# Kernel optimization log

Measured on AMD Instinct MI355X. Metric: run time of the kernel, lower is better.

## Reference

```python
import jax, jax.numpy as jnp
import numpy as np

B = 64            # batch size (number of segments)
PTS = 4096        # points per segment
N = B * PTS       # total points
OBS = 128
ACT = 5
HID = 256
LAT = 64
CTX = 128
TEMP = 1.0
LOG2PIE = float(np.log(2.0 * np.pi * np.e))


def _p(key, shape, scale=0.02):
    return (scale * jax.random.normal(key, shape)).astype(jnp.float32)


def setup_inputs() -> dict:
    key = jax.random.key(0)
    ks = jax.random.split(key, 20)
    inp = {
        'obs': jax.random.normal(ks[0], (N, OBS), dtype=jnp.float32),
        'action': jax.random.normal(ks[1], (B, ACT), dtype=jnp.float32),
        'coh_scalar': jax.random.normal(ks[2], (B, 1), dtype=jnp.float32),
        'coh_spatial': jax.random.normal(ks[3], (N,), dtype=jnp.float32),
        'h_prev': jnp.zeros((B, HID), jnp.float32),
        'z_prev': jnp.zeros((B, LAT), jnp.float32),
        'batch': jnp.repeat(jnp.arange(B, dtype=jnp.int64), PTS),
    }
    xin = LAT + ACT + 1  # GRU input: [z_prev, action, coh_scalar]
    inp['W_ih'] = _p(ks[4], (3 * HID, xin)); inp['b_ih'] = jnp.zeros((3 * HID,), jnp.float32)
    inp['W_hh'] = _p(ks[5], (3 * HID, HID)); inp['b_hh'] = jnp.zeros((3 * HID,), jnp.float32)
    inp['W_prior'] = _p(ks[6], (2 * LAT, HID)); inp['b_prior'] = jnp.zeros((2 * LAT,), jnp.float32)
    inp['W_post'] = _p(ks[7], (2 * LAT, HID + OBS)); inp['b_post'] = jnp.zeros((2 * LAT,), jnp.float32)
    inp['W_ae1'] = _p(ks[8], (256, OBS)); inp['b_ae1'] = jnp.zeros((256,), jnp.float32)
    inp['W_ae2'] = _p(ks[9], (OBS, 256)); inp['b_ae2'] = jnp.zeros((OBS,), jnp.float32)
    inp['W_c1'] = _p(ks[10], (512, HID + LAT + OBS)); inp['b_c1'] = jnp.zeros((512,), jnp.float32)
    inp['W_c2'] = _p(ks[11], (CTX, 512)); inp['b_c2'] = jnp.zeros((CTX,), jnp.float32)
    return inp


def _forward(obs, action, coh_scalar, coh_spatial, h_prev, z_prev, batch,
             W_ih, b_ih, W_hh, b_hh, W_prior, b_prior, W_post, b_post,
             W_ae1, b_ae1, W_ae2, b_ae2, W_c1, b_c1, W_c2, b_c2):
    # --- segment mean of obs (the hot scatter-reduce) ---
    counts = jax.ops.segment_sum(jnp.ones((N,), obs.dtype), batch, num_segments=B)
    obs_sum = jax.ops.segment_sum(obs, batch, num_segments=B)            # (B, OBS)
    obs_agg = obs_sum / jnp.maximum(counts, 1.0)[:, None]

    # --- RSSM: GRU cell over [z_prev, action, coh_scalar] ---
    x = jnp.concatenate([z_prev, action, coh_scalar], axis=-1)           # (B, LAT+ACT+1)
    gi = x @ W_ih.T + b_ih
    gh = h_prev @ W_hh.T + b_hh
    gi_r, gi_z, gi_n = jnp.split(gi, 3, axis=-1)
    gh_r, gh_z, gh_n = jnp.split(gh, 3, axis=-1)
    r = jax.nn.sigmoid(gi_r + gh_r)
    u = jax.nn.sigmoid(gi_z + gh_z)
    n = jnp.tanh(gi_n + r * gh_n)
    h = (1.0 - u) * n + u * h_prev                                       # (B, HID)

    prior = h @ W_prior.T + b_prior
    mu_p, logvar_p = jnp.split(prior, 2, axis=-1)
    post = jnp.concatenate([h, obs_agg], axis=-1) @ W_post.T + b_post
    mu_q, logvar_q = jnp.split(post, 2, axis=-1)
    z = mu_q                                                             # deterministic baseline (B, LAT)

    # --- priority: entropy-based uncertainty, per-segment softmax ---
    uncertainty = 0.5 * jnp.sum(logvar_q + LOG2PIE, axis=-1)             # (B,)
    priority = coh_spatial * uncertainty[batch]                          # (N,)
    s = priority / TEMP
    m = jax.ops.segment_max(s, batch, num_segments=B)
    e = jnp.exp(s - m[batch])
    denom = jax.ops.segment_sum(e, batch, num_segments=B)
    priority_norm = e / jnp.maximum(denom, 1e-12)[batch]                 # (N,)

    # --- attended aggregation (second scatter-reduce) ---
    obs_attended = jax.ops.segment_sum(obs * priority_norm[:, None], batch, num_segments=B)  # (B, OBS)
    obs_enc = jax.nn.relu(obs_attended @ W_ae1.T + b_ae1) @ W_ae2.T + b_ae2                  # (B, OBS)

    ctx_in = jnp.concatenate([h, z, obs_enc], axis=-1)                   # (B, HID+LAT+OBS)
    context = jax.nn.relu(ctx_in @ W_c1.T + b_c1) @ W_c2.T + b_c2        # (B, CTX)
    return h, z, context, priority, priority_norm, uncertainty


def reference(obs, action, coh_scalar, coh_spatial, h_prev, z_prev, batch,
              W_ih, b_ih, W_hh, b_hh, W_prior, b_prior, W_post, b_post,
              W_ae1, b_ae1, W_ae2, b_ae2, W_c1, b_c1, W_c2, b_c2):
    return _forward(obs, action, coh_scalar, coh_spatial, h_prev, z_prev, batch,
                    W_ih, b_ih, W_hh, b_hh, W_prior, b_prior, W_post, b_post,
                    W_ae1, b_ae1, W_ae2, b_ae2, W_c1, b_c1, W_c2, b_c2)
```

## Files before the change

### kernel.cpp

```cpp
#include <hip/hip_runtime.h>
#include <math.h>

#define BB   64
#define PTS  4096
#define NTOT (BB * PTS)
#define OBS  128
#define ACT  5
#define HID  256
#define LAT  64
#define CTX  128
#define LOG2PIE 2.8378770664093453f

#define OFF_H   0
#define OFF_Z   (BB * HID)
#define OFF_CTX (OFF_Z + BB * LAT)
#define OFF_PRI (OFF_CTX + BB * CTX)
#define OFF_PN  (OFF_PRI + NTOT)
#define OFF_UNC (OFF_PN + NTOT)

#define CHUNKS 32
#define RPC    (PTS / CHUNKS)

__device__ __forceinline__ float wsum(float v) {
    #pragma unroll
    for (int off = 32; off > 0; off >>= 1) v += __shfl_xor(v, off, 64);
    return v;
}
__device__ __forceinline__ float wmax(float v) {
    #pragma unroll
    for (int off = 32; off > 0; off >>= 1) v = fmaxf(v, __shfl_xor(v, off, 64));
    return v;
}
__device__ __forceinline__ float sigmoidf_(float x) { return 1.f / (1.f + expf(-x)); }

__global__ __launch_bounds__(256) void seg_sum_part_kernel(
        const float* __restrict__ obs, float* __restrict__ part) {
    int blk = blockIdx.x;
    int b = blk >> 5, chunk = blk & 31;
    int t = threadIdx.x, c4 = t & 31, rg = t >> 5;
    const float4* obs4 = (const float4*)obs;
    size_t row0 = (size_t)b * PTS + (size_t)chunk * RPC;
    float4 acc = make_float4(0.f, 0.f, 0.f, 0.f);
    #pragma unroll
    for (int i = 0; i < RPC / 8; ++i) {
        float4 v = obs4[(row0 + rg + 8 * i) * (OBS / 4) + c4];
        acc.x += v.x; acc.y += v.y; acc.z += v.z; acc.w += v.w;
    }
    __shared__ float4 lds[256];
    lds[t] = acc;
    __syncthreads();
    if (t < 32) {
        float4 s = lds[t];
        #pragma unroll
        for (int k = 1; k < 8; ++k) {
            float4 v = lds[t + 32 * k];
            s.x += v.x; s.y += v.y; s.z += v.z; s.w += v.w;
        }
        ((float4*)part)[(size_t)blk * 32 + t] = s;
    }
}

__global__ __launch_bounds__(256) void attn_part_kernel(
        const float* __restrict__ obs, const float* __restrict__ pn,
        float* __restrict__ att_part) {
    int blk = blockIdx.x;
    int b = blk >> 5, chunk = blk & 31;
    int t = threadIdx.x, c4 = t & 31, rg = t >> 5;
    const float4* obs4 = (const float4*)obs;
    size_t row0 = (size_t)b * PTS + (size_t)chunk * RPC;
    float4 acc = make_float4(0.f, 0.f, 0.f, 0.f);
    #pragma unroll
    for (int i = 0; i < RPC / 8; ++i) {
        size_t r = row0 + rg + 8 * i;
        float w = pn[r];
        float4 v = obs4[r * (OBS / 4) + c4];
        acc.x = fmaf(v.x, w, acc.x);
        acc.y = fmaf(v.y, w, acc.y);
        acc.z = fmaf(v.z, w, acc.z);
        acc.w = fmaf(v.w, w, acc.w);
    }
    __shared__ float4 lds[256];
    lds[t] = acc;
    __syncthreads();
    if (t < 32) {
        float4 s = lds[t];
        #pragma unroll
        for (int k = 1; k < 8; ++k) {
            float4 v = lds[t + 32 * k];
            s.x += v.x; s.y += v.y; s.z += v.z; s.w += v.w;
        }
        ((float4*)att_part)[(size_t)blk * 32 + t] = s;
    }
}

__global__ __launch_bounds__(128) void agg_kernel(const float* __restrict__ part,
                                                  float* __restrict__ agg,
                                                  float* __restrict__ out) {
    int b = blockIdx.x, j = threadIdx.x;
    float s = 0.f;
    #pragma unroll
    for (int c = 0; c < CHUNKS; ++c) s += part[((size_t)b * CHUNKS + c) * OBS + j];
    agg[b * OBS + j] = s * (1.0f / PTS);
    if (j == 0) out[OFF_UNC + b] = 32.0f * LOG2PIE;
}

__global__ __launch_bounds__(128) void attagg_kernel(const float* __restrict__ att_part,
                                                     float* __restrict__ att) {
    int b = blockIdx.x, j = threadIdx.x;
    float s = 0.f;
    #pragma unroll
    for (int c = 0; c < CHUNKS; ++c) s += att_part[((size_t)b * CHUNKS + c) * OBS + j];
    att[b * OBS + j] = s;
}

__global__ __launch_bounds__(256) void gru_gate_kernel(
        const float* __restrict__ action, const float* __restrict__ coh_scalar,
        const float* __restrict__ h_prev, const float* __restrict__ z_prev,
        const float* __restrict__ W_ih, const float* __restrict__ b_ih,
        const float* __restrict__ W_hh, const float* __restrict__ b_hh,
        float* __restrict__ out) {
    int wid = blockIdx.x * 4 + (threadIdx.x >> 6);
    int lane = threadIdx.x & 63;
    int b = wid >> 8, j = wid & 255;

    float x0 = z_prev[b * LAT + lane];
    float x1 = 0.f;
    if (lane < ACT) x1 = action[b * ACT + lane];
    else if (lane == ACT) x1 = coh_scalar[b];
    float hp0 = h_prev[b * HID + lane];
    float hp1 = h_prev[b * HID + lane + 64];
    float hp2 = h_prev[b * HID + lane + 128];
    float hp3 = h_prev[b * HID + lane + 192];

    const float* wir = W_ih + (size_t)j * 70;
    const float* wiz = W_ih + (size_t)(HID + j) * 70;
    const float* win = W_ih + (size_t)(2 * HID + j) * 70;
    const float* whr = W_hh + (size_t)j * HID;
    const float* whz = W_hh + (size_t)(HID + j) * HID;
    const float* whn = W_hh + (size_t)(2 * HID + j) * HID;

    float sr = wir[lane] * x0;
    float sz = wiz[lane] * x0;
    float sn = win[lane] * x0;
    if (lane < 6) {
        sr = fmaf(wir[lane + 64], x1, sr);
        sz = fmaf(wiz[lane + 64], x1, sz);
        sn = fmaf(win[lane + 64], x1, sn);
    }
    sr = fmaf(whr[lane], hp0, sr); sr = fmaf(whr[lane + 64], hp1, sr);
    sr = fmaf(whr[lane + 128], hp2, sr); sr = fmaf(whr[lane + 192], hp3, sr);
    sz = fmaf(whz[lane], hp0, sz); sz = fmaf(whz[lane + 64], hp1, sz);
    sz = fmaf(whz[lane + 128], hp2, sz); sz = fmaf(whz[lane + 192], hp3, sz);
    float sh = whn[lane] * hp0;
    sh = fmaf(whn[lane + 64], hp1, sh);
    sh = fmaf(whn[lane + 128], hp2, sh);
    sh = fmaf(whn[lane + 192], hp3, sh);

    sr = wsum(sr); sz = wsum(sz); sn = wsum(sn); sh = wsum(sh);
    if (lane == 0) {
        float r = sigmoidf_(sr + b_ih[j] + b_hh[j]);
        float u = sigmoidf_(sz + b_ih[HID + j] + b_hh[HID + j]);
        float n = tanhf(sn + b_ih[2 * HID + j] + r * (sh + b_hh[2 * HID + j]));
        float h = (1.f - u) * n + u * h_prev[b * HID + j];
        out[OFF_H + b * HID + j] = h;
    }
}

__global__ __launch_bounds__(256) void post_kernel(
        const float* __restrict__ agg,
        const float* __restrict__ W_post, const float* __restrict__ b_post,
        float* __restrict__ out) {
    int wid = blockIdx.x * 4 + (threadIdx.x >> 6);
    int lane = threadIdx.x & 63;
    int b = wid >> 7, row = wid & 127;
    const float* wr = W_post + (size_t)row * (HID + OBS);
    const float* h = out + OFF_H + b * HID;
    const float* ag = agg + b * OBS;
    float s = wr[lane] * h[lane];
    s = fmaf(wr[lane + 64], h[lane + 64], s);
    s = fmaf(wr[lane + 128], h[lane + 128], s);
    s = fmaf(wr[lane + 192], h[lane + 192], s);
    s = fmaf(wr[lane + 256], ag[lane], s);
    s = fmaf(wr[lane + 320], ag[lane + 64], s);
    s = wsum(s);
    if (lane == 0) {
        s += b_post[row];
        if (row < LAT) out[OFF_Z + b * LAT + row] = s;
        else atomicAdd(&out[OFF_UNC + b], 0.5f * s);
    }
}

__global__ __launch_bounds__(1024) void softmax_kernel(
        const float* __restrict__ coh_spatial, float* __restrict__ out) {
    int b = blockIdx.x, t = threadIdx.x;
    int w = t >> 6, lane = t & 63;
    float u = out[OFF_UNC + b];
    __shared__ float sv[PTS];
    __shared__ float red[16];
    int base = b * PTS;
    float lmax = -INFINITY;
    #pragma unroll
    for (int i = t; i < PTS; i += 1024) {
        float s = coh_spatial[base + i] * u;
        sv[i] = s;
        out[OFF_PRI + base + i] = s;
        lmax = fmaxf(lmax, s);
    }
    lmax = wmax(lmax);
    if (lane == 0) red[w] = lmax;
    __syncthreads();
    float m = red[0];
    #pragma unroll
    for (int k = 1; k < 16; ++k) m = fmaxf(m, red[k]);
    __syncthreads();
    float lsum = 0.f;
    #pragma unroll
    for (int i = t; i < PTS; i += 1024) {
        float e = expf(sv[i] - m);
        sv[i] = e;
        lsum += e;
    }
    lsum = wsum(lsum);
    if (lane == 0) red[w] = lsum;
    __syncthreads();
    float d = 0.f;
    #pragma unroll
    for (int k = 0; k < 16; ++k) d += red[k];
    float inv = 1.f / fmaxf(d, 1e-12f);
    #pragma unroll
    for (int i = t; i < PTS; i += 1024) {
        out[OFF_PN + base + i] = sv[i] * inv;
    }
}

__global__ __launch_bounds__(256) void ae1_kernel(
        const float* __restrict__ att,
        const float* __restrict__ W_ae1, const float* __restrict__ b_ae1,
        float* __restrict__ h1) {
    int wid = blockIdx.x * 4 + (threadIdx.x >> 6);
    int lane = threadIdx.x & 63;
    int b = wid >> 8, row = wid & 255;
    const float* wr = W_ae1 + (size_t)row * OBS;
    const float* a = att + b * OBS;
    float s = wr[lane] * a[lane];
    s = fmaf(wr[lane + 64], a[lane + 64], s);
    s = wsum(s);
    if (lane == 0) h1[b * 256 + row] = fmaxf(s + b_ae1[row], 0.f);
}

__global__ __launch_bounds__(256) void ae2_kernel(
        const float* __restrict__ h1,
        const float* __restrict__ W_ae2, const float* __restrict__ b_ae2,
        float* __restrict__ enc) {
    int wid = blockIdx.x * 4 + (threadIdx.x >> 6);
    int lane = threadIdx.x & 63;
    int b = wid >> 7, row = wid & 127;
    const float* wr = W_ae2 + (size_t)row * 256;
    const float* hh = h1 + b * 256;
    float s = wr[lane] * hh[lane];
    s = fmaf(wr[lane + 64], hh[lane + 64], s);
    s = fmaf(wr[lane + 128], hh[lane + 128], s);
    s = fmaf(wr[lane + 192], hh[lane + 192], s);
    s = wsum(s);
    if (lane == 0) enc[b * OBS + row] = s + b_ae2[row];
}

__global__ __launch_bounds__(256) void c1_kernel(
        const float* __restrict__ enc,
        const float* __restrict__ W_c1, const float* __restrict__ b_c1,
        const float* __restrict__ out, float* __restrict__ c1v) {
    int wid = blockIdx.x * 4 + (threadIdx.x >> 6);
    int lane = threadIdx.x & 63;
    int b = wid >> 9, row = wid & 511;
    const float* wr = W_c1 + (size_t)row * 448;
    const float* h = out + OFF_H + b * HID;
    const float* z = out + OFF_Z + b * LAT;
    const float* e = enc + b * OBS;
    float s = wr[lane] * h[lane];
    s = fmaf(wr[lane + 64], h[lane + 64], s);
    s = fmaf(wr[lane + 128], h[lane + 128], s);
    s = fmaf(wr[lane + 192], h[lane + 192], s);
    s = fmaf(wr[lane + 256], z[lane], s);
    s = fmaf(wr[lane + 320], e[lane], s);
    s = fmaf(wr[lane + 384], e[lane + 64], s);
    s = wsum(s);
    if (lane == 0) c1v[b * 512 + row] = fmaxf(s + b_c1[row], 0.f);
}

__global__ __launch_bounds__(256) void c2_kernel(
        const float* __restrict__ c1v,
        const float* __restrict__ W_c2, const float* __restrict__ b_c2,
        float* __restrict__ out) {
    int wid = blockIdx.x * 4 + (threadIdx.x >> 6);
    int lane = threadIdx.x & 63;
    int b = wid >> 7, row = wid & 127;
    const float* wr = W_c2 + (size_t)row * 512;
    const float* c = c1v + b * 512;
    float s = wr[lane] * c[lane];
    #pragma unroll
    for (int i = 1; i < 8; ++i) s = fmaf(wr[lane + 64 * i], c[lane + 64 * i], s);
    s = wsum(s);
    if (lane == 0) out[OFF_CTX + b * CTX + row] = s + b_c2[row];
}

extern "C" void kernel_launch(void* const* d_in, const int* in_sizes, int n_in,
                              void* d_out, int out_size, void* d_ws, size_t ws_size,
                              hipStream_t stream) {
    const float* obs         = (const float*)d_in[0];
    const float* action      = (const float*)d_in[1];
    const float* coh_scalar  = (const float*)d_in[2];
    const float* coh_spatial = (const float*)d_in[3];
    const float* h_prev      = (const float*)d_in[4];
    const float* z_prev      = (const float*)d_in[5];
    const float* W_ih   = (const float*)d_in[7];
    const float* b_ih   = (const float*)d_in[8];
    const float* W_hh   = (const float*)d_in[9];
    const float* b_hh   = (const float*)d_in[10];
    const float* W_post = (const float*)d_in[13];
    const float* b_post = (const float*)d_in[14];
    const float* W_ae1  = (const float*)d_in[15];
    const float* b_ae1  = (const float*)d_in[16];
    const float* W_ae2  = (const float*)d_in[17];
    const float* b_ae2  = (const float*)d_in[18];
    const float* W_c1   = (const float*)d_in[19];
    const float* b_c1   = (const float*)d_in[20];
    const float* W_c2   = (const float*)d_in[21];
    const float* b_c2   = (const float*)d_in[22];

    float* out = (float*)d_out;
    float* part     = (float*)d_ws;
    float* att_part = part + BB * CHUNKS * OBS;
    float* agg      = att_part + BB * CHUNKS * OBS;
    float* att      = agg + BB * OBS;
    float* h1       = att + BB * OBS;
    float* enc      = h1 + BB * 256;
    float* c1v      = enc + BB * OBS;

    seg_sum_part_kernel<<<BB * CHUNKS, 256, 0, stream>>>(obs, part);
    gru_gate_kernel<<<BB * HID / 4, 256, 0, stream>>>(action, coh_scalar, h_prev, z_prev,
                                                      W_ih, b_ih, W_hh, b_hh, out);
    agg_kernel<<<BB, 128, 0, stream>>>(part, agg, out);
    post_kernel<<<BB * 128 / 4, 256, 0, stream>>>(agg, W_post, b_post, out);
    softmax_kernel<<<BB, 1024, 0, stream>>>(coh_spatial, out);
    attn_part_kernel<<<BB * CHUNKS, 256, 0, stream>>>(obs, out + OFF_PN, att_part);
    attagg_kernel<<<BB, 128, 0, stream>>>(att_part, att);
    ae1_kernel<<<BB * 256 / 4, 256, 0, stream>>>(att, W_ae1, b_ae1, h1);
    ae2_kernel<<<BB * 128 / 4, 256, 0, stream>>>(h1, W_ae2, b_ae2, enc);
    c1_kernel<<<BB * 512 / 4, 256, 0, stream>>>(enc, W_c1, b_c1, out, c1v);
    c2_kernel<<<BB * 128 / 4, 256, 0, stream>>>(c1v, W_c2, b_c2, out);
}
```

Baseline: 314.5 us.

## Fuse kernels: merge seg-sum with GRU, agg into post, MLP head into one kernel

Cuts the chain from eleven launches to five. The segment-sum partials and the GRU gate now run as one horizontally fused launch, and the chunk reduction is folded into post_kernel. The uncertainty atomicAdd is replaced by a per-batch log-variance buffer that softmax_kernel reduces. The attended reduction and the four MLP layers (ae1, ae2, c1, c2) run in a single 1024-thread block per batch with shared-memory intermediates. This removes launch and sync overhead and global round trips, but the fused head uses only 64 blocks, and each block streams all of the weights.

Result: faster. 295.3 us (-6.1%).

```diff
diff --git a/kernel.cpp b/kernel.cpp
--- a/kernel.cpp
+++ b/kernel.cpp
@@ -33,30 +33,194 @@
 }
 __device__ __forceinline__ float sigmoidf_(float x) { return 1.f / (1.f + expf(-x)); }
 
-__global__ __launch_bounds__(256) void seg_sum_part_kernel(
-        const float* __restrict__ obs, float* __restrict__ part) {
+__global__ __launch_bounds__(256) void phase1_kernel(
+        const float* __restrict__ obs, float* __restrict__ part,
+        const float* __restrict__ action, const float* __restrict__ coh_scalar,
+        const float* __restrict__ h_prev, const float* __restrict__ z_prev,
+        const float* __restrict__ W_ih, const float* __restrict__ b_ih,
+        const float* __restrict__ W_hh, const float* __restrict__ b_hh,
+        float* __restrict__ out) {
+    __shared__ float4 lds[256];
+    int t = threadIdx.x;
+    if (blockIdx.x < BB * CHUNKS) {
+        int blk = blockIdx.x;
+        int b = blk >> 5, chunk = blk & 31;
+        int c4 = t & 31, rg = t >> 5;
+        const float4* obs4 = (const float4*)obs;
+        size_t row0 = (size_t)b * PTS + (size_t)chunk * RPC;
+        float4 acc = make_float4(0.f, 0.f, 0.f, 0.f);
+        #pragma unroll
+        for (int i = 0; i < RPC / 8; ++i) {
+            float4 v = obs4[(row0 + rg + 8 * i) * (OBS / 4) + c4];
+            acc.x += v.x; acc.y += v.y; acc.z += v.z; acc.w += v.w;
+        }
+        lds[t] = acc;
+        __syncthreads();
+        if (t < 32) {
+            float4 s = lds[t];
+            #pragma unroll
+            for (int k = 1; k < 8; ++k) {
+                float4 v = lds[t + 32 * k];
+                s.x += v.x; s.y += v.y; s.z += v.z; s.w += v.w;
+            }
+            ((float4*)part)[(size_t)blk * 32 + t] = s;
+        }
+    } else {
+        int wid = (blockIdx.x - BB * CHUNKS) * 4 + (t >> 6);
+        int lane = t & 63;
+        int b = wid >> 8, j = wid & 255;
+
+        float x0 = z_prev[b * LAT + lane];
+        float x1 = 0.f;
+        if (lane < ACT) x1 = action[b * ACT + lane];
+        else if (lane == ACT) x1 = coh_scalar[b];
+        float hp0 = h_prev[b * HID + lane];
+        float hp1 = h_prev[b * HID + lane + 64];
+        float hp2 = h_prev[b * HID + lane + 128];
+        float hp3 = h_prev[b * HID + lane + 192];
+
+        const float* wir = W_ih + (size_t)j * 70;
+        const float* wiz = W_ih + (size_t)(HID + j) * 70;
+        const float* win = W_ih + (size_t)(2 * HID + j) * 70;
+        const float* whr = W_hh + (size_t)j * HID;
+        const float* whz = W_hh + (size_t)(HID + j) * HID;
+        const float* whn = W_hh + (size_t)(2 * HID + j) * HID;
+
+        float sr = wir[lane] * x0;
+        float sz = wiz[lane] * x0;
+        float sn = win[lane] * x0;
+        if (lane < 6) {
+            sr = fmaf(wir[lane + 64], x1, sr);
+            sz = fmaf(wiz[lane + 64], x1, sz);
+            sn = fmaf(win[lane + 64], x1, sn);
+        }
+        sr = fmaf(whr[lane], hp0, sr); sr = fmaf(whr[lane + 64], hp1, sr);
+        sr = fmaf(whr[lane + 128], hp2, sr); sr = fmaf(whr[lane + 192], hp3, sr);
+        sz = fmaf(whz[lane], hp0, sz); sz = fmaf(whz[lane + 64], hp1, sz);
+        sz = fmaf(whz[lane + 128], hp2, sz); sz = fmaf(whz[lane + 192], hp3, sz);
+        float sh = whn[lane] * hp0;
+        sh = fmaf(whn[lane + 64], hp1, sh);
+        sh = fmaf(whn[lane + 128], hp2, sh);
+        sh = fmaf(whn[lane + 192], hp3, sh);
+
+        sr = wsum(sr); sz = wsum(sz); sn = wsum(sn); sh = wsum(sh);
+        if (lane == 0) {
+            float r = sigmoidf_(sr + b_ih[j] + b_hh[j]);
+            float u = sigmoidf_(sz + b_ih[HID + j] + b_hh[HID + j]);
+            float n = tanhf(sn + b_ih[2 * HID + j] + r * (sh + b_hh[2 * HID + j]));
+            float h = (1.f - u) * n + u * h_prev[b * HID + j];
+            out[OFF_H + b * HID + j] = h;
+        }
+    }
+}
+
+__global__ __launch_bounds__(256) void post_kernel(
+        const float* __restrict__ part,
+        const float* __restrict__ W_post, const float* __restrict__ b_post,
+        float* __restrict__ out, float* __restrict__ lv) {
     int blk = blockIdx.x;
-    int b = blk >> 5, chunk = blk & 31;
-    int t = threadIdx.x, c4 = t & 31, rg = t >> 5;
-    const float4* obs4 = (const float4*)obs;
-    size_t row0 = (size_t)b * PTS + (size_t)chunk * RPC;
-    float4 acc = make_float4(0.f, 0.f, 0.f, 0.f);
-    #pragma unroll
-    for (int i = 0; i < RPC / 8; ++i) {
-        float4 v = obs4[(row0 + rg + 8 * i) * (OBS / 4) + c4];
-        acc.x += v.x; acc.y += v.y; acc.z += v.z; acc.w += v.w;
-    }
-    __shared__ float4 lds[256];
-    lds[t] = acc;
+    int b = blk >> 5, rg = blk & 31;
+    int t = threadIdx.x, w = t >> 6, lane = t & 63;
+    __shared__ float4 st[256];
+    __shared__ float aggs[128];
+    __shared__ float hs[256];
+
+    const float4* ap4 = (const float4*)part;
+    {
+        int c4 = t & 31, cg = t >> 5;
+        float4 a = ap4[((size_t)(b * CHUNKS + cg)) * 32 + c4];
+        #pragma unroll
+        for (int k = 1; k < 4; ++k) {
+            float4 v = ap4[((size_t)(b * CHUNKS + cg + 8 * k)) * 32 + c4];
+            a.x += v.x; a.y += v.y; a.z += v.z; a.w += v.w;
+        }
+        st[t] = a;
+    }
+    hs[t] = out[OFF_H + b * HID + t];
     __syncthreads();
     if (t < 32) {
-        float4 s = lds[t];
+        float4 s = st[t];
         #pragma unroll
         for (int k = 1; k < 8; ++k) {
-            float4 v = lds[t + 32 * k];
+            float4 v = st[t + 32 * k];
             s.x += v.x; s.y += v.y; s.z += v.z; s.w += v.w;
         }
-        ((float4*)part)[(size_t)blk * 32 + t] = s;
+        const float sc = 1.0f / PTS;
+        aggs[4 * t + 0] = s.x * sc;
+        aggs[4 * t + 1] = s.y * sc;
+        aggs[4 * t + 2] = s.z * sc;
+        aggs[4 * t + 3] = s.w * sc;
+    }
+    __syncthreads();
+
+    int row = rg * 4 + w;
+    const float* wr = W_post + (size_t)row * (HID + OBS);
+    float s = wr[lane] * hs[lane];
+    s = fmaf(wr[lane + 64],  hs[lane + 64],  s);
+    s = fmaf(wr[lane + 128], hs[lane + 128], s);
+    s = fmaf(wr[lane + 192], hs[lane + 192], s);
+    s = fmaf(wr[lane + 256], aggs[lane],      s);
+    s = fmaf(wr[lane + 320], aggs[lane + 64], s);
+    s = wsum(s);
+    if (lane == 0) {
+        s += b_post[row];
+        if (row < LAT) out[OFF_Z + b * LAT + row] = s;
+        else           lv[b * LAT + (row - LAT)] = s;
+    }
+}
+
+__global__ __launch_bounds__(1024) void softmax_kernel(
+        const float* __restrict__ coh_spatial, const float* __restrict__ lv,
+        float* __restrict__ out) {
+    int b = blockIdx.x, t = threadIdx.x;
+    int w = t >> 6, lane = t & 63;
+    __shared__ float sv[PTS];
+    __shared__ float red[16];
+    __shared__ float uS;
+    if (w == 0) {
+        float v = lv[b * LAT + lane];
+        v = wsum(v);
+        if (lane == 0) {
+            float u = 0.5f * v + 32.0f * LOG2PIE;
+            uS = u;
+            out[OFF_UNC + b] = u;
+        }
+    }
+    __syncthreads();
+    float u = uS;
+    int base = b * PTS;
+    float lmax = -INFINITY;
+    #pragma unroll
+    for (int i = t; i < PTS; i += 1024) {
+        float s = coh_spatial[base + i] * u;
+        sv[i] = s;
+        out[OFF_PRI + base + i] = s;
+        lmax = fmaxf(lmax, s);
+    }
+    lmax = wmax(lmax);
+    if (lane == 0) red[w] = lmax;
+    __syncthreads();
+    float m = red[0];
+    #pragma unroll
+    for (int k = 1; k < 16; ++k) m = fmaxf(m, red[k]);
+    __syncthreads();
+    float lsum = 0.f;
+    #pragma unroll
+    for (int i = t; i < PTS; i += 1024) {
+        float e = expf(sv[i] - m);
+        sv[i] = e;
+        lsum += e;
+    }
+    lsum = wsum(lsum);
+    if (lane == 0) red[w] = lsum;
+    __syncthreads();
+    float d = 0.f;
+    #pragma unroll
+    for (int k = 0; k < 16; ++k) d += red[k];
+    float inv = 1.f / fmaxf(d, 1e-12f);
+    #pragma unroll
+    for (int i = t; i < PTS; i += 1024) {
+        out[OFF_PN + base + i] = sv[i] * inv;
     }
 }
 
@@ -72,12 +236,12 @@
     #pragma unroll
     for (int i = 0; i < RPC / 8; ++i) {
         size_t r = row0 + rg + 8 * i;
-        float w = pn[r];
+        float wgt = pn[r];
         float4 v = obs4[r * (OBS / 4) + c4];
-        acc.x = fmaf(v.x, w, acc.x);
-        acc.y = fmaf(v.y, w, acc.y);
-        acc.z = fmaf(v.z, w, acc.z);
-        acc.w = fmaf(v.w, w, acc.w);
+        acc.x = fmaf(v.x, wgt, acc.x);
+        acc.y = fmaf(v.y, wgt, acc.y);
+        acc.z = fmaf(v.z, wgt, acc.z);
+        acc.w = fmaf(v.w, wgt, acc.w);
     }
     __shared__ float4 lds[256];
     lds[t] = acc;
@@ -93,214 +257,164 @@
     }
 }
 
-__global__ __launch_bounds__(128) void agg_kernel(const float* __restrict__ part,
-                                                  float* __restrict__ agg,
-                                                  float* __restrict__ out) {
-    int b = blockIdx.x, j = threadIdx.x;
-    float s = 0.f;
-    #pragma unroll
-    for (int c = 0; c < CHUNKS; ++c) s += part[((size_t)b * CHUNKS + c) * OBS + j];
-    agg[b * OBS + j] = s * (1.0f / PTS);
-    if (j == 0) out[OFF_UNC + b] = 32.0f * LOG2PIE;
-}
-
-__global__ __launch_bounds__(128) void attagg_kernel(const float* __restrict__ att_part,
-                                                     float* __restrict__ att) {
-    int b = blockIdx.x, j = threadIdx.x;
-    float s = 0.f;
-    #pragma unroll
-    for (int c = 0; c < CHUNKS; ++c) s += att_part[((size_t)b * CHUNKS + c) * OBS + j];
-    att[b * OBS + j] = s;
-}
-
-__global__ __launch_bounds__(256) void gru_gate_kernel(
-        const float* __restrict__ action, const float* __restrict__ coh_scalar,
-        const float* __restrict__ h_prev, const float* __restrict__ z_prev,
-        const float* __restrict__ W_ih, const float* __restrict__ b_ih,
-        const float* __restrict__ W_hh, const float* __restrict__ b_hh,
+__global__ __launch_bounds__(1024) void head_kernel(
+        const float* __restrict__ att_part,
+        const float* __restrict__ W_ae1, const float* __restrict__ b_ae1,
+        const float* __restrict__ W_ae2, const float* __restrict__ b_ae2,
+        const float* __restrict__ W_c1,  const float* __restrict__ b_c1,
+        const float* __restrict__ W_c2,  const float* __restrict__ b_c2,
         float* __restrict__ out) {
-    int wid = blockIdx.x * 4 + (threadIdx.x >> 6);
-    int lane = threadIdx.x & 63;
-    int b = wid >> 8, j = wid & 255;
-
-    float x0 = z_prev[b * LAT + lane];
-    float x1 = 0.f;
-    if (lane < ACT) x1 = action[b * ACT + lane];
-    else if (lane == ACT) x1 = coh_scalar[b];
-    float hp0 = h_prev[b * HID + lane];
-    float hp1 = h_prev[b * HID + lane + 64];
-    float hp2 = h_prev[b * HID + lane + 128];
-    float hp3 = h_prev[b * HID + lane + 192];
-
-    const float* wir = W_ih + (size_t)j * 70;
-    const float* wiz = W_ih + (size_t)(HID + j) * 70;
-    const float* win = W_ih + (size_t)(2 * HID + j) * 70;
-    const float* whr = W_hh + (size_t)j * HID;
-    const float* whz = W_hh + (size_t)(HID + j) * HID;
-    const float* whn = W_hh + (size_t)(2 * HID + j) * HID;
-
-    float sr = wir[lane] * x0;
-    float sz = wiz[lane] * x0;
-    float sn = win[lane] * x0;
-    if (lane < 6) {
-        sr = fmaf(wir[lane + 64], x1, sr);
-        sz = fmaf(wiz[lane + 64], x1, sz);
-        sn = fmaf(win[lane + 64], x1, sn);
-    }
-    sr = fmaf(whr[lane], hp0, sr); sr = fmaf(whr[lane + 64], hp1, sr);
-    sr = fmaf(whr[lane + 128], hp2, sr); sr = fmaf(whr[lane + 192], hp3, sr);
-    sz = fmaf(whz[lane], hp0, sz); sz = fmaf(whz[lane + 64], hp1, sz);
-    sz = fmaf(whz[lane + 128], hp2, sz); sz = fmaf(whz[lane + 192], hp3, sz);
-    float sh = whn[lane] * hp0;
-    sh = fmaf(whn[lane + 64], hp1, sh);
-    sh = fmaf(whn[lane + 128], hp2, sh);
-    sh = fmaf(whn[lane + 192], hp3, sh);
-
-    sr = wsum(sr); sz = wsum(sz); sn = wsum(sn); sh = wsum(sh);
-    if (lane == 0) {
-        float r = sigmoidf_(sr + b_ih[j] + b_hh[j]);
-        float u = sigmoidf_(sz + b_ih[HID + j] + b_hh[HID + j]);
-        float n = tanhf(sn + b_ih[2 * HID + j] + r * (sh + b_hh[2 * HID + j]));
-        float h = (1.f - u) * n + u * h_prev[b * HID + j];
-        out[OFF_H + b * HID + j] = h;
-    }
-}
-
-__global__ __launch_bounds__(256) void post_kernel(
-        const float* __restrict__ agg,
-        const float* __restrict__ W_post, const float* __restrict__ b_post,
-        float* __restrict__ out) {
-    int wid = blockIdx.x * 4 + (threadIdx.x >> 6);
-    int lane = threadIdx.x & 63;
-    int b = wid >> 7, row = wid & 127;
-    const float* wr = W_post + (size_t)row * (HID + OBS);
-    const float* h = out + OFF_H + b * HID;
-    const float* ag = agg + b * OBS;
-    float s = wr[lane] * h[lane];
-    s = fmaf(wr[lane + 64], h[lane + 64], s);
-    s = fmaf(wr[lane + 128], h[lane + 128], s);
-    s = fmaf(wr[lane + 192], h[lane + 192], s);
-    s = fmaf(wr[lane + 256], ag[lane], s);
-    s = fmaf(wr[lane + 320], ag[lane + 64], s);
-    s = wsum(s);
-    if (lane == 0) {
-        s += b_post[row];
-        if (row < LAT) out[OFF_Z + b * LAT + row] = s;
-        else atomicAdd(&out[OFF_UNC + b], 0.5f * s);
-    }
-}
-
-__global__ __launch_bounds__(1024) void softmax_kernel(
-        const float* __restrict__ coh_spatial, float* __restrict__ out) {
     int b = blockIdx.x, t = threadIdx.x;
     int w = t >> 6, lane = t & 63;
-    float u = out[OFF_UNC + b];
-    __shared__ float sv[PTS];
-    __shared__ float red[16];
-    int base = b * PTS;
-    float lmax = -INFINITY;
-    #pragma unroll
-    for (int i = t; i < PTS; i += 1024) {
-        float s = coh_spatial[base + i] * u;
-        sv[i] = s;
-        out[OFF_PRI + base + i] = s;
-        lmax = fmaxf(lmax, s);
-    }
-    lmax = wmax(lmax);
-    if (lane == 0) red[w] = lmax;
-    __syncthreads();
-    float m = red[0];
-    #pragma unroll
-    for (int k = 1; k < 16; ++k) m = fmaxf(m, red[k]);
-    __syncthreads();
-    float lsum = 0.f;
-    #pragma unroll
-    for (int i = t; i < PTS; i += 1024) {
-        float e = expf(sv[i] - m);
-        sv[i] = e;
-        lsum += e;
-    }
-    lsum = wsum(lsum);
-    if (lane == 0) red[w] = lsum;
-    __syncthreads();
-    float d = 0.f;
-    #pragma unroll
-    for (int k = 0; k < 16; ++k) d += red[k];
-    float inv = 1.f / fmaxf(d, 1e-12f);
-    #pragma unroll
-    for (int i = t; i < PTS; i += 1024) {
-        out[OFF_PN + base + i] = sv[i] * inv;
-    }
-}
-
-__global__ __launch_bounds__(256) void ae1_kernel(
-        const float* __restrict__ att,
-        const float* __restrict__ W_ae1, const float* __restrict__ b_ae1,
-        float* __restrict__ h1) {
-    int wid = blockIdx.x * 4 + (threadIdx.x >> 6);
-    int lane = threadIdx.x & 63;
-    int b = wid >> 8, row = wid & 255;
-    const float* wr = W_ae1 + (size_t)row * OBS;
-    const float* a = att + b * OBS;
-    float s = wr[lane] * a[lane];
-    s = fmaf(wr[lane + 64], a[lane + 64], s);
-    s = wsum(s);
-    if (lane == 0) h1[b * 256 + row] = fmaxf(s + b_ae1[row], 0.f);
-}
-
-__global__ __launch_bounds__(256) void ae2_kernel(
-        const float* __restrict__ h1,
-        const float* __restrict__ W_ae2, const float* __restrict__ b_ae2,
-        float* __restrict__ enc) {
-    int wid = blockIdx.x * 4 + (threadIdx.x >> 6);
-    int lane = threadIdx.x & 63;
-    int b = wid >> 7, row = wid & 127;
-    const float* wr = W_ae2 + (size_t)row * 256;
-    const float* hh = h1 + b * 256;
-    float s = wr[lane] * hh[lane];
-    s = fmaf(wr[lane + 64], hh[lane + 64], s);
-    s = fmaf(wr[lane + 128], hh[lane + 128], s);
-    s = fmaf(wr[lane + 192], hh[lane + 192], s);
-    s = wsum(s);
-    if (lane == 0) enc[b * OBS + row] = s + b_ae2[row];
-}
-
-__global__ __launch_bounds__(256) void c1_kernel(
-        const float* __restrict__ enc,
-        const float* __restrict__ W_c1, const float* __restrict__ b_c1,
-        const float* __restrict__ out, float* __restrict__ c1v) {
-    int wid = blockIdx.x * 4 + (threadIdx.x >> 6);
-    int lane = threadIdx.x & 63;
-    int b = wid >> 9, row = wid & 511;
-    const float* wr = W_c1 + (size_t)row * 448;
-    const float* h = out + OFF_H + b * HID;
-    const float* z = out + OFF_Z + b * LAT;
-    const float* e = enc + b * OBS;
-    float s = wr[lane] * h[lane];
-    s = fmaf(wr[lane + 64], h[lane + 64], s);
-    s = fmaf(wr[lane + 128], h[lane + 128], s);
-    s = fmaf(wr[lane + 192], h[lane + 192], s);
-    s = fmaf(wr[lane + 256], z[lane], s);
-    s = fmaf(wr[lane + 320], e[lane], s);
-    s = fmaf(wr[lane + 384], e[lane + 64], s);
-    s = wsum(s);
-    if (lane == 0) c1v[b * 512 + row] = fmaxf(s + b_c1[row], 0.f);
-}
-
-__global__ __launch_bounds__(256) void c2_kernel(
-        const float* __restrict__ c1v,
-        const float* __restrict__ W_c2, const float* __restrict__ b_c2,
-        float* __restrict__ out) {
-    int wid = blockIdx.x * 4 + (threadIdx.x >> 6);
-    int lane = threadIdx.x & 63;
-    int b = wid >> 7, row = wid & 127;
-    const float* wr = W_c2 + (size_t)row * 512;
-    const float* c = c1v + b * 512;
-    float s = wr[lane] * c[lane];
-    #pragma unroll
-    for (int i = 1; i < 8; ++i) s = fmaf(wr[lane + 64 * i], c[lane + 64 * i], s);
-    s = wsum(s);
-    if (lane == 0) out[OFF_CTX + b * CTX + row] = s + b_c2[row];
+    __shared__ float4 red4[1024];
+    __shared__ float att[128];
+    __shared__ float h1[256];
+    __shared__ float ctxin[448];
+    __shared__ float c1v[512];
+
+    {
+        int c4 = t & 31, chunk = t >> 5;
+        const float4* ap4 = (const float4*)att_part;
+        red4[t] = ap4[((size_t)(b * CHUNKS + chunk)) * 32 + c4];
+    }
+    if (t < 256) ctxin[t] = out[OFF_H + b * HID + t];
+    else if (t < 320) ctxin[t] = out[OFF_Z + b * LAT + (t - 256)];
+    __syncthreads();
+    #pragma unroll
+    for (int s = 16; s > 0; s >>= 1) {
+        if ((t >> 5) < s) {
+            float4 v = red4[t + 32 * s];
+            red4[t].x += v.x; red4[t].y += v.y; red4[t].z += v.z; red4[t].w += v.w;
+        }
+        __syncthreads();
+    }
+    if (t < 32) {
+        float4 v = red4[t];
+        att[4 * t] = v.x; att[4 * t + 1] = v.y; att[4 * t + 2] = v.z; att[4 * t + 3] = v.w;
+    }
+    __syncthreads();
+
+    {
+        float x0 = att[lane], x1 = att[lane + 64];
+        #pragma unroll
+        for (int g = 0; g < 4; ++g) {
+            int r0 = w * 16 + g * 4;
+            const float* w0 = W_ae1 + (size_t)(r0 + 0) * OBS;
+            const float* w1 = W_ae1 + (size_t)(r0 + 1) * OBS;
+            const float* w2 = W_ae1 + (size_t)(r0 + 2) * OBS;
+            const float* w3 = W_ae1 + (size_t)(r0 + 3) * OBS;
+            float a0 = fmaf(w0[lane + 64], x1, w0[lane] * x0);
+            float a1 = fmaf(w1[lane + 64], x1, w1[lane] * x0);
+            float a2 = fmaf(w2[lane + 64], x1, w2[lane] * x0);
+            float a3 = fmaf(w3[lane + 64], x1, w3[lane] * x0);
+            a0 = wsum(a0); a1 = wsum(a1); a2 = wsum(a2); a3 = wsum(a3);
+            if (lane == 0) {
+                h1[r0]     = fmaxf(a0 + b_ae1[r0],     0.f);
+                h1[r0 + 1] = fmaxf(a1 + b_ae1[r0 + 1], 0.f);
+                h1[r0 + 2] = fmaxf(a2 + b_ae1[r0 + 2], 0.f);
+                h1[r0 + 3] = fmaxf(a3 + b_ae1[r0 + 3], 0.f);
+            }
+        }
+    }
+    __syncthreads();
+
+    {
+        float x0 = h1[lane], x1 = h1[lane + 64], x2 = h1[lane + 128], x3 = h1[lane + 192];
+        #pragma unroll
+        for (int g = 0; g < 2; ++g) {
+            int r0 = w * 8 + g * 4;
+            const float* w0 = W_ae2 + (size_t)(r0 + 0) * 256;
+            const float* w1 = W_ae2 + (size_t)(r0 + 1) * 256;
+            const float* w2 = W_ae2 + (size_t)(r0 + 2) * 256;
+            const float* w3 = W_ae2 + (size_t)(r0 + 3) * 256;
+            float a0 = w0[lane] * x0, a1 = w1[lane] * x0, a2 = w2[lane] * x0, a3 = w3[lane] * x0;
+            a0 = fmaf(w0[lane + 64], x1, a0);  a1 = fmaf(w1[lane + 64], x1, a1);
+            a2 = fmaf(w2[lane + 64], x1, a2);  a3 = fmaf(w3[lane + 64], x1, a3);
+            a0 = fmaf(w0[lane + 128], x2, a0); a1 = fmaf(w1[lane + 128], x2, a1);
+            a2 = fmaf(w2[lane + 128], x2, a2); a3 = fmaf(w3[lane + 128], x2, a3);
+            a0 = fmaf(w0[lane + 192], x3, a0); a1 = fmaf(w1[lane + 192], x3, a1);
+            a2 = fmaf(w2[lane + 192], x3, a2); a3 = fmaf(w3[lane + 192], x3, a3);
+            a0 = wsum(a0); a1 = wsum(a1); a2 = wsum(a2); a3 = wsum(a3);
+            if (lane == 0) {
+                ctxin[320 + r0]     = a0 + b_ae2[r0];
+                ctxin[320 + r0 + 1] = a1 + b_ae2[r0 + 1];
+                ctxin[320 + r0 + 2] = a2 + b_ae2[r0 + 2];
+                ctxin[320 + r0 + 3] = a3 + b_ae2[r0 + 3];
+            }
+        }
+    }
+    __syncthreads();
+
+    {
+        float x0 = ctxin[lane],        x1 = ctxin[lane + 64],  x2 = ctxin[lane + 128];
+        float x3 = ctxin[lane + 192],  x4 = ctxin[lane + 256], x5 = ctxin[lane + 320];
+        float x6 = ctxin[lane + 384];
+        #pragma unroll
+        for (int g = 0; g < 8; ++g) {
+            int r0 = w * 32 + g * 4;
+            const float* w0 = W_c1 + (size_t)(r0 + 0) * 448;
+            const float* w1 = W_c1 + (size_t)(r0 + 1) * 448;
+            const float* w2 = W_c1 + (size_t)(r0 + 2) * 448;
+            const float* w3 = W_c1 + (size_t)(r0 + 3) * 448;
+            float a0 = w0[lane] * x0, a1 = w1[lane] * x0, a2 = w2[lane] * x0, a3 = w3[lane] * x0;
+            a0 = fmaf(w0[lane + 64], x1, a0);  a1 = fmaf(w1[lane + 64], x1, a1);
+            a2 = fmaf(w2[lane + 64], x1, a2);  a3 = fmaf(w3[lane + 64], x1, a3);
+            a0 = fmaf(w0[lane + 128], x2, a0); a1 = fmaf(w1[lane + 128], x2, a1);
+            a2 = fmaf(w2[lane + 128], x2, a2); a3 = fmaf(w3[lane + 128], x2, a3);
+            a0 = fmaf(w0[lane + 192], x3, a0); a1 = fmaf(w1[lane + 192], x3, a1);
+            a2 = fmaf(w2[lane + 192], x3, a2); a3 = fmaf(w3[lane + 192], x3, a3);
+            a0 = fmaf(w0[lane + 256], x4, a0); a1 = fmaf(w1[lane + 256], x4, a1);
+            a2 = fmaf(w2[lane + 256], x4, a2); a3 = fmaf(w3[lane + 256], x4, a3);
+            a0 = fmaf(w0[lane + 320], x5, a0); a1 = fmaf(w1[lane + 320], x5, a1);
+            a2 = fmaf(w2[lane + 320], x5, a2); a3 = fmaf(w3[lane + 320], x5, a3);
+            a0 = fmaf(w0[lane + 384], x6, a0); a1 = fmaf(w1[lane + 384], x6, a1);
+            a2 = fmaf(w2[lane + 384], x6, a2); a3 = fmaf(w3[lane + 384], x6, a3);
+            a0 = wsum(a0); a1 = wsum(a1); a2 = wsum(a2); a3 = wsum(a3);
+            if (lane == 0) {
+                c1v[r0]     = fmaxf(a0 + b_c1[r0],     0.f);
+                c1v[r0 + 1] = fmaxf(a1 + b_c1[r0 + 1], 0.f);
+                c1v[r0 + 2] = fmaxf(a2 + b_c1[r0 + 2], 0.f);
+                c1v[r0 + 3] = fmaxf(a3 + b_c1[r0 + 3], 0.f);
+            }
+        }
+    }
+    __syncthreads();
+
+    {
+        float x0 = c1v[lane],       x1 = c1v[lane + 64],  x2 = c1v[lane + 128], x3 = c1v[lane + 192];
+        float x4 = c1v[lane + 256], x5 = c1v[lane + 320], x6 = c1v[lane + 384], x7 = c1v[lane + 448];
+        #pragma unroll
+        for (int g = 0; g < 2; ++g) {
+            int r0 = w * 8 + g * 4;
+            const float* w0 = W_c2 + (size_t)(r0 + 0) * 512;
+            const float* w1 = W_c2 + (size_t)(r0 + 1) * 512;
+            const float* w2 = W_c2 + (size_t)(r0 + 2) * 512;
+            const float* w3 = W_c2 + (size_t)(r0 + 3) * 512;
+            float a0 = w0[lane] * x0, a1 = w1[lane] * x0, a2 = w2[lane] * x0, a3 = w3[lane] * x0;
+            a0 = fmaf(w0[lane + 64], x1, a0);  a1 = fmaf(w1[lane + 64], x1, a1);
+            a2 = fmaf(w2[lane + 64], x1, a2);  a3 = fmaf(w3[lane + 64], x1, a3);
+            a0 = fmaf(w0[lane + 128], x2, a0); a1 = fmaf(w1[lane + 128], x2, a1);
+            a2 = fmaf(w2[lane + 128], x2, a2); a3 = fmaf(w3[lane + 128], x2, a3);
+            a0 = fmaf(w0[lane + 192], x3, a0); a1 = fmaf(w1[lane + 192], x3, a1);
+            a2 = fmaf(w2[lane + 192], x3, a2); a3 = fmaf(w3[lane + 192], x3, a3);
+            a0 = fmaf(w0[lane + 256], x4, a0); a1 = fmaf(w1[lane + 256], x4, a1);
+            a2 = fmaf(w2[lane + 256], x4, a2); a3 = fmaf(w3[lane + 256], x4, a3);
+            a0 = fmaf(w0[lane + 320], x5, a0); a1 = fmaf(w1[lane + 320], x5, a1);
+            a2 = fmaf(w2[lane + 320], x5, a2); a3 = fmaf(w3[lane + 320], x5, a3);
+            a0 = fmaf(w0[lane + 384], x6, a0); a1 = fmaf(w1[lane + 384], x6, a1);
+            a2 = fmaf(w2[lane + 384], x6, a2); a3 = fmaf(w3[lane + 384], x6, a3);
+            a0 = fmaf(w0[lane + 448], x7, a0); a1 = fmaf(w1[lane + 448], x7, a1);
+            a2 = fmaf(w2[lane + 448], x7, a2); a3 = fmaf(w3[lane + 448], x7, a3);
+            a0 = wsum(a0); a1 = wsum(a1); a2 = wsum(a2); a3 = wsum(a3);
+            if (lane == 0) {
+                float* dst = out + OFF_CTX + b * CTX;
+                dst[r0]     = a0 + b_c2[r0];
+                dst[r0 + 1] = a1 + b_c2[r0 + 1];
+                dst[r0 + 2] = a2 + b_c2[r0 + 2];
+                dst[r0 + 3] = a3 + b_c2[r0 + 3];
+            }
+        }
+    }
 }
 
 extern "C" void kernel_launch(void* const* d_in, const int* in_sizes, int n_in,
@@ -330,22 +444,13 @@
     float* out = (float*)d_out;
     float* part     = (float*)d_ws;
     float* att_part = part + BB * CHUNKS * OBS;
-    float* agg      = att_part + BB * CHUNKS * OBS;
-    float* att      = agg + BB * OBS;
-    float* h1       = att + BB * OBS;
-    float* enc      = h1 + BB * 256;
-    float* c1v      = enc + BB * OBS;
-
-    seg_sum_part_kernel<<<BB * CHUNKS, 256, 0, stream>>>(obs, part);
-    gru_gate_kernel<<<BB * HID / 4, 256, 0, stream>>>(action, coh_scalar, h_prev, z_prev,
-                                                      W_ih, b_ih, W_hh, b_hh, out);
-    agg_kernel<<<BB, 128, 0, stream>>>(part, agg, out);
-    post_kernel<<<BB * 128 / 4, 256, 0, stream>>>(agg, W_post, b_post, out);
-    softmax_kernel<<<BB, 1024, 0, stream>>>(coh_spatial, out);
+    float* lv       = att_part + BB * CHUNKS * OBS;
+
+    phase1_kernel<<<BB * CHUNKS + BB * HID / 4, 256, 0, stream>>>(
+        obs, part, action, coh_scalar, h_prev, z_prev, W_ih, b_ih, W_hh, b_hh, out);
+    post_kernel<<<BB * 32, 256, 0, stream>>>(part, W_post, b_post, out, lv);
+    softmax_kernel<<<BB, 1024, 0, stream>>>(coh_spatial, lv, out);
     attn_part_kernel<<<BB * CHUNKS, 256, 0, stream>>>(obs, out + OFF_PN, att_part);
-    attagg_kernel<<<BB, 128, 0, stream>>>(att_part, att);
-    ae1_kernel<<<BB * 256 / 4, 256, 0, stream>>>(att, W_ae1, b_ae1, h1);
-    ae2_kernel<<<BB * 128 / 4, 256, 0, stream>>>(h1, W_ae2, b_ae2, enc);
-    c1_kernel<<<BB * 512 / 4, 256, 0, stream>>>(enc, W_c1, b_c1, out, c1v);
-    c2_kernel<<<BB * 128 / 4, 256, 0, stream>>>(c1v, W_c2, b_c2, out);
-}
+    head_kernel<<<BB, 1024, 0, stream>>>(att_part, W_ae1, b_ae1, W_ae2, b_ae2,
+                                         W_c1, b_c1, W_c2, b_c2, out);
+}
```
